# Optimization experiments

Hardware: AMD Instinct MI355X
Metric: run time of the kernel (lower is better)

## Reference

```python
import jax, jax.numpy as jnp
import numpy as np

EMB = 1024
HEADS = 16
HEAD_DIM = EMB // HEADS
BLOCK = 256
N_GLOBAL = 4
WINDOW = 128
ROPE_BASE = 10000.0


def rotate_half(x):
    # interleaved rotate: (-x2_0, x1_0, -x2_1, x1_1, ...), faithful to source
    x1 = x[..., ::2]
    x2 = x[..., 1::2]
    return jnp.stack((-x2, x1), axis=-1).reshape(x.shape)


def setup_inputs() -> dict:
    key = jax.random.key(0)
    k0, k1, k2 = jax.random.split(key, 3)
    B, S = 2, 2048
    x = jax.random.normal(k0, (B, S, EMB), dtype=jnp.float32)
    # Linear weights stored as [in, out]; y = x @ W (bias=False in source)
    w_qkv = jax.random.normal(k1, (EMB, 3 * EMB), dtype=jnp.float32) * (EMB ** -0.5)
    w_out = jax.random.normal(k2, (EMB, EMB), dtype=jnp.float32) * (EMB ** -0.5)
    return {"x": x, "w_qkv": w_qkv, "w_out": w_out}


def _forward(x, w_qkv, w_out):
    B, S, E = x.shape
    H, D = HEADS, HEAD_DIM
    qkv = (x @ w_qkv).reshape(B, S, 3, H, D).transpose(2, 0, 3, 1, 4)  # [3,B,H,S,D]
    q, k, v = qkv[0], qkv[1], qkv[2]

    # Rotary embedding (start_pos = 0, no cache)
    inv_freq = 1.0 / (ROPE_BASE ** (jnp.arange(0, D, 2, dtype=jnp.float32) / D))
    pos = jnp.arange(S, dtype=jnp.float32)
    freqs = jnp.outer(pos, inv_freq)                 # [S, D/2]
    emb = jnp.concatenate([freqs, freqs], axis=-1)   # [S, D]
    cos = jnp.cos(emb)[None, None]                   # [1,1,S,D]
    sin = jnp.sin(emb)[None, None]
    q = q * cos + rotate_half(q) * sin
    k = k * cos + rotate_half(k) * sin

    # Block-local + global-token + sliding-window mask, AND causal (vectorized)
    i = jnp.arange(S)[:, None]
    j = jnp.arange(S)[None, :]
    allowed = (i // BLOCK == j // BLOCK) | (i < N_GLOBAL) | (j < N_GLOBAL) \
              | (jnp.abs(i - j) <= WINDOW)
    allowed = allowed & (j <= i)
    # NOTE: source passes ~mask to F.scaled_dot_product_attention, where a
    # boolean attn_mask with True means "attend". We replicate that exactly.
    attend = ~allowed  # [S, S]

    scale = D ** -0.5
    scores = jnp.einsum("bhsd,bhtd->bhst", q, k) * scale      # [B,H,S,S]
    scores = jnp.where(attend[None, None], scores, jnp.float32(-1e30))
    attn = jax.nn.softmax(scores, axis=-1)
    out = jnp.einsum("bhst,bhtd->bhsd", attn, v)              # [B,H,S,D]
    out = out.transpose(0, 2, 1, 3).reshape(B, S, E)
    return out @ w_out


def reference(x, w_qkv, w_out):
    return _forward(x, w_qkv, w_out)
```

## Files before the change

### kernel.cpp

```cpp
#include <hip/hip_runtime.h>
#include <hip/hip_bf16.h>

#define EMBD   1024
#define NHEAD  16
#define HDIM   64
#define SEQ    2048
#define BATCH  2
#define MROWS  4096
#define NQKV   3072
#define VSTR   2064

using floatx4 = __attribute__((ext_vector_type(4))) float;
using short8  = __attribute__((ext_vector_type(8))) short;

static __device__ __forceinline__ float bf2f(unsigned short u) {
    unsigned int v = ((unsigned int)u) << 16;
    return __uint_as_float(v);
}
static __device__ __forceinline__ unsigned short f2bf(float f) {
    __hip_bfloat16 h = __float2bfloat16(f);
    return *reinterpret_cast<unsigned short*>(&h);
}

__global__ __launch_bounds__(256) void cast_x(
    const float* __restrict__ x, unsigned short* __restrict__ xh,
    unsigned short* __restrict__ xl)
{
    int idx = (blockIdx.x * 256 + threadIdx.x) * 4;
    float4 v = *(const float4*)(x + idx);
    ushort4 h, l;
    h.x = f2bf(v.x); l.x = f2bf(v.x - bf2f(h.x));
    h.y = f2bf(v.y); l.y = f2bf(v.y - bf2f(h.y));
    h.z = f2bf(v.z); l.z = f2bf(v.z - bf2f(h.z));
    h.w = f2bf(v.w); l.w = f2bf(v.w - bf2f(h.w));
    *(ushort4*)(xh + idx) = h;
    *(ushort4*)(xl + idx) = l;
}

__global__ __launch_bounds__(256) void cast_wT(
    const float* __restrict__ w, unsigned short* __restrict__ wT, int N)
{
    __shared__ unsigned short th[64][65];
    const int k0 = blockIdx.y * 64, n0 = blockIdx.x * 64;
    const int t = threadIdx.x;
    const int r = t >> 4, c = (t & 15) * 4;
    for (int rr = r; rr < 64; rr += 16) {
        float4 v = *(const float4*)(w + (size_t)(k0 + rr) * N + n0 + c);
        th[rr][c + 0] = f2bf(v.x);
        th[rr][c + 1] = f2bf(v.y);
        th[rr][c + 2] = f2bf(v.z);
        th[rr][c + 3] = f2bf(v.w);
    }
    __syncthreads();
    for (int rr = r; rr < 64; rr += 16) {
        ushort4 h;
        h.x = th[c + 0][rr]; h.y = th[c + 1][rr];
        h.z = th[c + 2][rr]; h.w = th[c + 3][rr];
        *(ushort4*)(wT + (size_t)(n0 + rr) * 1024 + k0 + c) = h;
    }
}

__global__ __launch_bounds__(256) void gemm_qkv_mfma(
    const unsigned short* __restrict__ xh, const unsigned short* __restrict__ xl,
    const unsigned short* __restrict__ wbT,
    unsigned short* __restrict__ qst, unsigned short* __restrict__ kst,
    unsigned short* __restrict__ vtT)
{
    const int t = threadIdx.x, wave = t >> 6, lane = t & 63;
    const int col = lane & 15, quad = lane >> 4;
    const int n0 = blockIdx.x * 128;
    const int m0 = blockIdx.y * 128;
    const int which = n0 >> 10;
    const int wm = (wave >> 1) * 64, wn = (wave & 1) * 64;

    floatx4 acc[4][4];
    #pragma unroll
    for (int i = 0; i < 4; ++i)
        #pragma unroll
        for (int j = 0; j < 4; ++j) acc[i][j] = (floatx4){0.f, 0.f, 0.f, 0.f};

    const unsigned short* pa_h = xh  + (size_t)(m0 + wm + col) * 1024 + quad * 8;
    const unsigned short* pa_l = xl  + (size_t)(m0 + wm + col) * 1024 + quad * 8;
    const unsigned short* pb   = wbT + (size_t)(n0 + wn + col) * 1024 + quad * 8;

    for (int k0 = 0; k0 < 1024; k0 += 32) {
        short8 bf[4], ah[4], al[4];
        #pragma unroll
        for (int f = 0; f < 4; ++f) bf[f] = *(const short8*)(pb   + f * 16 * 1024 + k0);
        #pragma unroll
        for (int f = 0; f < 4; ++f) ah[f] = *(const short8*)(pa_h + f * 16 * 1024 + k0);
        #pragma unroll
        for (int f = 0; f < 4; ++f) al[f] = *(const short8*)(pa_l + f * 16 * 1024 + k0);

        if (which < 2) {
            #pragma unroll
            for (int fm = 0; fm < 4; ++fm)
                #pragma unroll
                for (int fn = 0; fn < 4; ++fn) {
                    acc[fm][fn] = __builtin_amdgcn_mfma_f32_16x16x32_bf16(
                        bf[fn], ah[fm], acc[fm][fn], 0, 0, 0);
                    acc[fm][fn] = __builtin_amdgcn_mfma_f32_16x16x32_bf16(
                        bf[fn], al[fm], acc[fm][fn], 0, 0, 0);
                }
        } else {
            #pragma unroll
            for (int fm = 0; fm < 4; ++fm)
                #pragma unroll
                for (int fn = 0; fn < 4; ++fn) {
                    acc[fm][fn] = __builtin_amdgcn_mfma_f32_16x16x32_bf16(
                        ah[fm], bf[fn], acc[fm][fn], 0, 0, 0);
                    acc[fm][fn] = __builtin_amdgcn_mfma_f32_16x16x32_bf16(
                        al[fm], bf[fn], acc[fm][fn], 0, 0, 0);
                }
        }
    }

    const float RLOG = 9.210340371976184f / 32.0f;
    if (which < 2) {
        unsigned short* dst = (which == 0) ? qst : kst;
        const float scale = (which == 0) ? 0.125f : 1.0f;
        #pragma unroll
        for (int fm = 0; fm < 4; ++fm) {
            const int s_g = m0 + wm + fm * 16 + col;
            const int b = s_g >> 11, s = s_g & 2047;
            const float sf = (float)s;
            #pragma unroll
            for (int fn = 0; fn < 4; ++fn) {
                const int nl = (n0 & 1023) + wn + fn * 16 + quad * 4;
                const int h = nl >> 6;
                const int d0 = nl & 63;
                floatx4 c = acc[fm][fn];
                float o_[4];
                #pragma unroll
                for (int pp = 0; pp < 2; ++pp) {
                    int de = d0 + pp * 2;
                    float fe = __expf(-(float)(de & 31) * RLOG);
                    float fo = __expf(-(float)((de + 1) & 31) * RLOG);
                    float se, ce, so, co;
                    sincosf(sf * fe, &se, &ce);
                    sincosf(sf * fo, &so, &co);
                    float qe = c[pp * 2], qo = c[pp * 2 + 1];
                    o_[pp * 2]     = (qe * ce - qo * se) * scale;
                    o_[pp * 2 + 1] = (qo * co + qe * so) * scale;
                }
                ushort4 o4;
                o4.x = f2bf(o_[0]); o4.y = f2bf(o_[1]);
                o4.z = f2bf(o_[2]); o4.w = f2bf(o_[3]);
                *(ushort4*)(dst + ((size_t)(b * 16 + h) * 2048 + s) * 64 + d0) = o4;
            }
        }
    } else {
        #pragma unroll
        for (int fm = 0; fm < 4; ++fm) {
            const int m = m0 + wm + fm * 16 + quad * 4;
            const int b = m >> 11, s0 = m & 2047;
            #pragma unroll
            for (int fn = 0; fn < 4; ++fn) {
                const int nl = (n0 & 1023) + wn + fn * 16 + col;
                const int h = nl >> 6;
                const int d = nl & 63;
                floatx4 c = acc[fm][fn];
                ushort4 o4;
                o4.x = f2bf(c[0]); o4.y = f2bf(c[1]);
                o4.z = f2bf(c[2]); o4.w = f2bf(c[3]);
                *(ushort4*)(vtT + (size_t)(b * 16 + h) * 64 * VSTR
                                + (size_t)d * VSTR + s0) = o4;
            }
        }
    }
}

__global__ __launch_bounds__(256) void attn_mfma(
    const unsigned short* __restrict__ qst,
    const unsigned short* __restrict__ kst,
    const unsigned short* __restrict__ vtT,
    unsigned short* __restrict__ attn)
{
    __shared__ unsigned short p_tile[4][16][32];
    __shared__ float4 redbuf[3][64][5];

    const int tid  = threadIdx.x;
    const int wave = tid >> 6;
    const int lane = tid & 63;
    const int col  = lane & 15;
    const int quad = lane >> 4;

    const int bh   = blockIdx.x >> 7;
    const int row0 = (blockIdx.x & 127) * 16;

    const size_t base  = (size_t)bh * SEQ * HDIM;
    const size_t vbase = (size_t)bh * HDIM * VSTR;

    const unsigned short* qp = qst + base + (size_t)(row0 + col) * HDIM + quad * 8;
    short8 aq0 = *(const short8*)(qp);
    short8 aq1 = *(const short8*)(qp + 32);

    int iR[4], ngR[4], j0R[4];
    #pragma unroll
    for (int r = 0; r < 4; ++r) {
        int i = row0 + quad * 4 + r;
        iR[r] = i;
        ngR[r] = (i + 1 < 4) ? (i + 1) : 4;
        int L = i - 128;
        int bs = (i >> 8) << 8;
        if (bs < L) L = bs;
        if (L < 0) L = 0;
        j0R[r] = (L > 4) ? L : 4;
    }

    floatx4 o0 = {0.f, 0.f, 0.f, 0.f}, o1 = o0, o2 = o0, o3 = o0;
    float lsum[4] = {0.f, 0.f, 0.f, 0.f};

    const int kbeg = wave * (SEQ / 4);
    for (int c32 = 0; c32 < (SEQ / 4) / 32; ++c32) {
        const int kc0 = kbeg + c32 * 32;
        #pragma unroll
        for (int h16 = 0; h16 < 2; ++h16) {
            const int kc = kc0 + h16 * 16;
            const unsigned short* kp = kst + base + (size_t)(kc + col) * HDIM + quad * 8;
            short8 bk0 = *(const short8*)(kp);
            short8 bk1 = *(const short8*)(kp + 32);
            floatx4 s = {0.f, 0.f, 0.f, 0.f};
            s = __builtin_amdgcn_mfma_f32_16x16x32_bf16(aq0, bk0, s, 0, 0, 0);
            s = __builtin_amdgcn_mfma_f32_16x16x32_bf16(aq1, bk1, s, 0, 0, 0);
            const int j = kc + col;
            #pragma unroll
            for (int r = 0; r < 4; ++r) {
                bool excl = (j < ngR[r]) || (j >= j0R[r] && j <= iR[r]);
                float p = excl ? 0.f : __expf(s[r]);
                lsum[r] += p;
                p_tile[wave][quad * 4 + r][h16 * 16 + col] = f2bf(p);
            }
        }
        short8 ap = *(const short8*)&p_tile[wave][col][quad * 8];
        const unsigned short* vp = vtT + vbase + (size_t)col * VSTR + kc0 + quad * 8;
        short8 bv0 = *(const short8*)(vp);
        short8 bv1 = *(const short8*)(vp + 16 * VSTR);
        short8 bv2 = *(const short8*)(vp + 32 * VSTR);
        short8 bv3 = *(const short8*)(vp + 48 * VSTR);
        o0 = __builtin_amdgcn_mfma_f32_16x16x32_bf16(ap, bv0, o0, 0, 0, 0);
        o1 = __builtin_amdgcn_mfma_f32_16x16x32_bf16(ap, bv1, o1, 0, 0, 0);
        o2 = __builtin_amdgcn_mfma_f32_16x16x32_bf16(ap, bv2, o2, 0, 0, 0);
        o3 = __builtin_amdgcn_mfma_f32_16x16x32_bf16(ap, bv3, o3, 0, 0, 0);
    }

    #pragma unroll
    for (int r = 0; r < 4; ++r) {
        float v = lsum[r];
        v += __shfl_xor(v, 1);
        v += __shfl_xor(v, 2);
        v += __shfl_xor(v, 4);
        v += __shfl_xor(v, 8);
        lsum[r] = v;
    }

    if (wave > 0) {
        redbuf[wave - 1][lane][0] = make_float4(o0[0], o0[1], o0[2], o0[3]);
        redbuf[wave - 1][lane][1] = make_float4(o1[0], o1[1], o1[2], o1[3]);
        redbuf[wave - 1][lane][2] = make_float4(o2[0], o2[1], o2[2], o2[3]);
        redbuf[wave - 1][lane][3] = make_float4(o3[0], o3[1], o3[2], o3[3]);
        redbuf[wave - 1][lane][4] = make_float4(lsum[0], lsum[1], lsum[2], lsum[3]);
    }
    __syncthreads();
    if (wave == 0) {
        #pragma unroll
        for (int w = 0; w < 3; ++w) {
            float4 t0 = redbuf[w][lane][0];
            float4 t1 = redbuf[w][lane][1];
            float4 t2 = redbuf[w][lane][2];
            float4 t3 = redbuf[w][lane][3];
            float4 tl = redbuf[w][lane][4];
            o0[0] += t0.x; o0[1] += t0.y; o0[2] += t0.z; o0[3] += t0.w;
            o1[0] += t1.x; o1[1] += t1.y; o1[2] += t1.z; o1[3] += t1.w;
            o2[0] += t2.x; o2[1] += t2.y; o2[2] += t2.z; o2[3] += t2.w;
            o3[0] += t3.x; o3[1] += t3.y; o3[2] += t3.z; o3[3] += t3.w;
            lsum[0] += tl.x; lsum[1] += tl.y; lsum[2] += tl.z; lsum[3] += tl.w;
        }
        const int b = bh >> 4, h = bh & 15;
        #pragma unroll
        for (int r = 0; r < 4; ++r) {
            float inv = 1.0f / lsum[r];
            unsigned short* orow = attn + ((size_t)(b * SEQ + iR[r])) * EMBD
                                        + h * HDIM + col;
            orow[0]  = f2bf(o0[r] * inv);
            orow[16] = f2bf(o1[r] * inv);
            orow[32] = f2bf(o2[r] * inv);
            orow[48] = f2bf(o3[r] * inv);
        }
    }
}

__global__ __launch_bounds__(256) void gemm_out_mfma(
    const unsigned short* __restrict__ A,
    const unsigned short* __restrict__ woT,
    float* __restrict__ out)
{
    const int t = threadIdx.x, wave = t >> 6, lane = t & 63;
    const int col = lane & 15, quad = lane >> 4;
    const int n0 = blockIdx.x * 128;
    const int m0 = blockIdx.y * 128;
    const int wm = (wave >> 1) * 64, wn = (wave & 1) * 64;

    floatx4 acc[4][4];
    #pragma unroll
    for (int i = 0; i < 4; ++i)
        #pragma unroll
        for (int j = 0; j < 4; ++j) acc[i][j] = (floatx4){0.f, 0.f, 0.f, 0.f};

    const unsigned short* pa = A   + (size_t)(m0 + wm + col) * 1024 + quad * 8;
    const unsigned short* pb = woT + (size_t)(n0 + wn + col) * 1024 + quad * 8;

    for (int k0 = 0; k0 < 1024; k0 += 32) {
        short8 af[4], bf[4];
        #pragma unroll
        for (int f = 0; f < 4; ++f) bf[f] = *(const short8*)(pb + f * 16 * 1024 + k0);
        #pragma unroll
        for (int f = 0; f < 4; ++f) af[f] = *(const short8*)(pa + f * 16 * 1024 + k0);
        #pragma unroll
        for (int fm = 0; fm < 4; ++fm)
            #pragma unroll
            for (int fn = 0; fn < 4; ++fn)
                acc[fm][fn] = __builtin_amdgcn_mfma_f32_16x16x32_bf16(
                    af[fm], bf[fn], acc[fm][fn], 0, 0, 0);
    }

    #pragma unroll
    for (int fm = 0; fm < 4; ++fm) {
        const int m = m0 + wm + fm * 16 + quad * 4;
        #pragma unroll
        for (int fn = 0; fn < 4; ++fn) {
            const int n = n0 + wn + fn * 16 + col;
            floatx4 c = acc[fm][fn];
            out[(size_t)(m + 0) * 1024 + n] = c[0];
            out[(size_t)(m + 1) * 1024 + n] = c[1];
            out[(size_t)(m + 2) * 1024 + n] = c[2];
            out[(size_t)(m + 3) * 1024 + n] = c[3];
        }
    }
}

extern "C" void kernel_launch(void* const* d_in, const int* in_sizes, int n_in,
                              void* d_out, int out_size, void* d_ws, size_t ws_size,
                              hipStream_t stream) {
    const float* x     = (const float*)d_in[0];
    const float* w_qkv = (const float*)d_in[1];
    const float* w_out = (const float*)d_in[2];
    float* out = (float*)d_out;

    unsigned short* ws16 = (unsigned short*)d_ws;
    unsigned short* xh  = ws16;
    unsigned short* xl  = ws16 +  4194304;
    unsigned short* wbT = ws16 +  8388608;
    unsigned short* woT = ws16 + 11534336;
    unsigned short* qst = ws16 + 12582912;
    unsigned short* kst = ws16 + 16777216;
    unsigned short* vtT = ws16 + 20971520;
    unsigned short* aws = ws16 + 25198592;

    dim3 blk(256);
    cast_x<<<dim3(4096), blk, 0, stream>>>(x, xh, xl);
    cast_wT<<<dim3(48, 16), blk, 0, stream>>>(w_qkv, wbT, NQKV);
    cast_wT<<<dim3(16, 16), blk, 0, stream>>>(w_out, woT, EMBD);

    gemm_qkv_mfma<<<dim3(NQKV / 128, MROWS / 128), blk, 0, stream>>>(
        xh, xl, wbT, qst, kst, vtT);

    attn_mfma<<<dim3(32 * 128), blk, 0, stream>>>(qst, kst, vtT, aws);

    gemm_out_mfma<<<dim3(EMBD / 128, MROWS / 128), blk, 0, stream>>>(aws, woT, out);
}
```

Baseline: 443.0 us.

## Compute transposed scores to keep P in registers and double-buffer K/V loads

The attention kernel now computes S^T (K as the A operand, Q as B) so each lane holds probabilities laid out as the A operand of a 16x16x16 bf16 MFMA. This removes the LDS round trip through p_tile used to transpose P before the PV product. K and V fragments for the next 32-key chunk are loaded into a second register buffer while the current chunk is computed, hiding global-load latency. The cost is higher register pressure, twice as many smaller PV MFMAs, and a shuffle-based redistribution of row sums at the end.

```diff
diff --git a/kernel.cpp b/kernel.cpp
--- a/kernel.cpp
+++ b/kernel.cpp
@@ -12,6 +12,7 @@
 
 using floatx4 = __attribute__((ext_vector_type(4))) float;
 using short8  = __attribute__((ext_vector_type(8))) short;
+using bshort4 = __attribute__((ext_vector_type(4))) short;
 
 static __device__ __forceinline__ float bf2f(unsigned short u) {
     unsigned int v = ((unsigned int)u) << 16;
@@ -20,6 +21,16 @@
 static __device__ __forceinline__ unsigned short f2bf(float f) {
     __hip_bfloat16 h = __float2bfloat16(f);
     return *reinterpret_cast<unsigned short*>(&h);
+}
+
+static __device__ __forceinline__ floatx4 mfma16x16x16bf16(bshort4 a, bshort4 b, floatx4 c) {
+#if __has_builtin(__builtin_amdgcn_mfma_f32_16x16x16bf16_1k)
+    return __builtin_amdgcn_mfma_f32_16x16x16bf16_1k(a, b, c, 0, 0, 0);
+#else
+    asm volatile("v_mfma_f32_16x16x16_bf16 %0, %1, %2, %0"
+                 : "+v"(c) : "v"(a), "v"(b));
+    return c;
+#endif
 }
 
 __global__ __launch_bounds__(256) void cast_x(
@@ -176,7 +187,6 @@
     const unsigned short* __restrict__ vtT,
     unsigned short* __restrict__ attn)
 {
-    __shared__ unsigned short p_tile[4][16][32];
     __shared__ float4 redbuf[3][64][5];
 
     const int tid  = threadIdx.x;
@@ -195,71 +205,93 @@
     short8 aq0 = *(const short8*)(qp);
     short8 aq1 = *(const short8*)(qp + 32);
 
-    int iR[4], ngR[4], j0R[4];
+    const int i_q = row0 + col;
+    const int ng  = (i_q + 1 < 4) ? (i_q + 1) : 4;
+    int L  = i_q - 128;
+    int bs = (i_q >> 8) << 8;
+    if (bs < L) L = bs;
+    if (L < 0) L = 0;
+    const int j0 = (L > 4) ? L : 4;
+
+    floatx4 o0 = {0.f, 0.f, 0.f, 0.f}, o1 = o0, o2 = o0, o3 = o0;
+    float lsum = 0.f;
+
+    const int kbeg = wave * (SEQ / 4);
+
+    short8  kf[2][4];
+    bshort4 vf[2][8];
+
+#define LOADKV(B, IT) do {                                                        \
+        const int kc_ = kbeg + (IT) * 32;                                         \
+        const unsigned short* kp_ = kst + base + (size_t)(kc_ + col) * HDIM       \
+                                        + quad * 8;                               \
+        kf[B][0] = *(const short8*)(kp_);                                         \
+        kf[B][1] = *(const short8*)(kp_ + 32);                                    \
+        kf[B][2] = *(const short8*)(kp_ + 16 * HDIM);                             \
+        kf[B][3] = *(const short8*)(kp_ + 16 * HDIM + 32);                        \
+        const unsigned short* vp_ = vtT + vbase + (size_t)col * VSTR              \
+                                        + kc_ + quad * 4;                         \
+        vf[B][0] = *(const bshort4*)(vp_);                                        \
+        vf[B][1] = *(const bshort4*)(vp_ + 16);                                   \
+        vf[B][2] = *(const bshort4*)(vp_ + 16 * VSTR);                            \
+        vf[B][3] = *(const bshort4*)(vp_ + 16 * VSTR + 16);                       \
+        vf[B][4] = *(const bshort4*)(vp_ + 32 * VSTR);                            \
+        vf[B][5] = *(const bshort4*)(vp_ + 32 * VSTR + 16);                       \
+        vf[B][6] = *(const bshort4*)(vp_ + 48 * VSTR);                            \
+        vf[B][7] = *(const bshort4*)(vp_ + 48 * VSTR + 16);                       \
+    } while (0)
+
+    LOADKV(0, 0);
     #pragma unroll
-    for (int r = 0; r < 4; ++r) {
-        int i = row0 + quad * 4 + r;
-        iR[r] = i;
-        ngR[r] = (i + 1 < 4) ? (i + 1) : 4;
-        int L = i - 128;
-        int bs = (i >> 8) << 8;
-        if (bs < L) L = bs;
-        if (L < 0) L = 0;
-        j0R[r] = (L > 4) ? L : 4;
-    }
-
-    floatx4 o0 = {0.f, 0.f, 0.f, 0.f}, o1 = o0, o2 = o0, o3 = o0;
-    float lsum[4] = {0.f, 0.f, 0.f, 0.f};
-
-    const int kbeg = wave * (SEQ / 4);
-    for (int c32 = 0; c32 < (SEQ / 4) / 32; ++c32) {
-        const int kc0 = kbeg + c32 * 32;
-        #pragma unroll
-        for (int h16 = 0; h16 < 2; ++h16) {
-            const int kc = kc0 + h16 * 16;
-            const unsigned short* kp = kst + base + (size_t)(kc + col) * HDIM + quad * 8;
-            short8 bk0 = *(const short8*)(kp);
-            short8 bk1 = *(const short8*)(kp + 32);
-            floatx4 s = {0.f, 0.f, 0.f, 0.f};
-            s = __builtin_amdgcn_mfma_f32_16x16x32_bf16(aq0, bk0, s, 0, 0, 0);
-            s = __builtin_amdgcn_mfma_f32_16x16x32_bf16(aq1, bk1, s, 0, 0, 0);
-            const int j = kc + col;
-            #pragma unroll
-            for (int r = 0; r < 4; ++r) {
-                bool excl = (j < ngR[r]) || (j >= j0R[r] && j <= iR[r]);
-                float p = excl ? 0.f : __expf(s[r]);
-                lsum[r] += p;
-                p_tile[wave][quad * 4 + r][h16 * 16 + col] = f2bf(p);
-            }
-        }
-        short8 ap = *(const short8*)&p_tile[wave][col][quad * 8];
-        const unsigned short* vp = vtT + vbase + (size_t)col * VSTR + kc0 + quad * 8;
-        short8 bv0 = *(const short8*)(vp);
-        short8 bv1 = *(const short8*)(vp + 16 * VSTR);
-        short8 bv2 = *(const short8*)(vp + 32 * VSTR);
-        short8 bv3 = *(const short8*)(vp + 48 * VSTR);
-        o0 = __builtin_amdgcn_mfma_f32_16x16x32_bf16(ap, bv0, o0, 0, 0, 0);
-        o1 = __builtin_amdgcn_mfma_f32_16x16x32_bf16(ap, bv1, o1, 0, 0, 0);
-        o2 = __builtin_amdgcn_mfma_f32_16x16x32_bf16(ap, bv2, o2, 0, 0, 0);
-        o3 = __builtin_amdgcn_mfma_f32_16x16x32_bf16(ap, bv3, o3, 0, 0, 0);
-    }
-
+    for (int it = 0; it < 16; ++it) {
+        const int cur = it & 1;
+        if (it < 15) LOADKV(cur ^ 1, it + 1);
+
+        floatx4 s0 = {0.f, 0.f, 0.f, 0.f}, s1 = s0;
+        s0 = __builtin_amdgcn_mfma_f32_16x16x32_bf16(kf[cur][0], aq0, s0, 0, 0, 0);
+        s0 = __builtin_amdgcn_mfma_f32_16x16x32_bf16(kf[cur][1], aq1, s0, 0, 0, 0);
+        s1 = __builtin_amdgcn_mfma_f32_16x16x32_bf16(kf[cur][2], aq0, s1, 0, 0, 0);
+        s1 = __builtin_amdgcn_mfma_f32_16x16x32_bf16(kf[cur][3], aq1, s1, 0, 0, 0);
+
+        const int kc = kbeg + it * 32;
+        bshort4 p0, p1;
+        #pragma unroll
+        for (int r = 0; r < 4; ++r) {
+            const int j1 = kc + quad * 4 + r;
+            const bool e1 = (j1 < ng) || (j1 >= j0 && j1 <= i_q);
+            const float pv1 = e1 ? 0.f : __expf(s0[r]);
+            lsum += pv1;
+            p0[r] = (short)f2bf(pv1);
+            const int j2 = j1 + 16;
+            const bool e2 = (j2 < ng) || (j2 >= j0 && j2 <= i_q);
+            const float pv2 = e2 ? 0.f : __expf(s1[r]);
+            lsum += pv2;
+            p1[r] = (short)f2bf(pv2);
+        }
+
+        o0 = mfma16x16x16bf16(p0, vf[cur][0], o0);
+        o0 = mfma16x16x16bf16(p1, vf[cur][1], o0);
+        o1 = mfma16x16x16bf16(p0, vf[cur][2], o1);
+        o1 = mfma16x16x16bf16(p1, vf[cur][3], o1);
+        o2 = mfma16x16x16bf16(p0, vf[cur][4], o2);
+        o2 = mfma16x16x16bf16(p1, vf[cur][5], o2);
+        o3 = mfma16x16x16bf16(p0, vf[cur][6], o3);
+        o3 = mfma16x16x16bf16(p1, vf[cur][7], o3);
+    }
+#undef LOADKV
+
+    lsum += __shfl_xor(lsum, 16);
+    lsum += __shfl_xor(lsum, 32);
+    float lsumR[4];
     #pragma unroll
-    for (int r = 0; r < 4; ++r) {
-        float v = lsum[r];
-        v += __shfl_xor(v, 1);
-        v += __shfl_xor(v, 2);
-        v += __shfl_xor(v, 4);
-        v += __shfl_xor(v, 8);
-        lsum[r] = v;
-    }
+    for (int r = 0; r < 4; ++r) lsumR[r] = __shfl(lsum, quad * 4 + r);
 
     if (wave > 0) {
         redbuf[wave - 1][lane][0] = make_float4(o0[0], o0[1], o0[2], o0[3]);
         redbuf[wave - 1][lane][1] = make_float4(o1[0], o1[1], o1[2], o1[3]);
         redbuf[wave - 1][lane][2] = make_float4(o2[0], o2[1], o2[2], o2[3]);
         redbuf[wave - 1][lane][3] = make_float4(o3[0], o3[1], o3[2], o3[3]);
-        redbuf[wave - 1][lane][4] = make_float4(lsum[0], lsum[1], lsum[2], lsum[3]);
+        redbuf[wave - 1][lane][4] = make_float4(lsumR[0], lsumR[1], lsumR[2], lsumR[3]);
     }
     __syncthreads();
     if (wave == 0) {
@@ -274,13 +306,14 @@
             o1[0] += t1.x; o1[1] += t1.y; o1[2] += t1.z; o1[3] += t1.w;
             o2[0] += t2.x; o2[1] += t2.y; o2[2] += t2.z; o2[3] += t2.w;
             o3[0] += t3.x; o3[1] += t3.y; o3[2] += t3.z; o3[3] += t3.w;
-            lsum[0] += tl.x; lsum[1] += tl.y; lsum[2] += tl.z; lsum[3] += tl.w;
+            lsumR[0] += tl.x; lsumR[1] += tl.y; lsumR[2] += tl.z; lsumR[3] += tl.w;
         }
         const int b = bh >> 4, h = bh & 15;
         #pragma unroll
         for (int r = 0; r < 4; ++r) {
-            float inv = 1.0f / lsum[r];
-            unsigned short* orow = attn + ((size_t)(b * SEQ + iR[r])) * EMBD
+            float inv = 1.0f / lsumR[r];
+            const int i_out = row0 + quad * 4 + r;
+            unsigned short* orow = attn + ((size_t)(b * SEQ + i_out)) * EMBD
                                         + h * HDIM + col;
             orow[0]  = f2bf(o0[r] * inv);
             orow[16] = f2bf(o1[r] * inv);
```

Result: slower. 471.6 us (+6.5%).
